# Performance work log

Hardware: AMD Instinct MI355X
Metric: run time of the kernel (lower is better)

## Reference

```python
import jax, jax.numpy as jnp
import numpy as np

B, Lq, C, NH, NP, DFF = 8, 10000, 256, 8, 4, 1024
H_IMG, W_IMG = 100, 100
HD = C // NH


def _layer_norm(x, g, b, eps=1e-5):
    m = jnp.mean(x, -1, keepdims=True)
    v = jnp.mean((x - m) ** 2, -1, keepdims=True)
    return (x - m) / jnp.sqrt(v + eps) * g + b


def _bilinear_sample(value, loc, Hs, Ws):
    # value: [B, Lin, NH, HD]; loc: [B, Lq, NH, NP, 2] normalized to [0,1]
    vt = jnp.transpose(value, (0, 2, 1, 3))  # [B, NH, Lin, HD]
    # move to [B, NH, Lq, NP] layout once; grid_sample(align_corners=False) pixel coords
    x = jnp.transpose(loc[..., 0], (0, 2, 1, 3)) * Ws - 0.5
    y = jnp.transpose(loc[..., 1], (0, 2, 1, 3)) * Hs - 0.5
    x0 = jnp.floor(x); y0 = jnp.floor(y)
    lx = x - x0; ly = y - y0

    def corner(xi, yi, w):
        valid = (xi >= 0) & (xi < Ws) & (yi >= 0) & (yi < Hs)
        xc = jnp.clip(xi, 0, Ws - 1).astype(jnp.int32)
        yc = jnp.clip(yi, 0, Hs - 1).astype(jnp.int32)
        idx = (yc * Ws + xc).reshape(B, NH, Lq * NP, 1)
        v = jnp.take_along_axis(vt, idx, axis=2).reshape(B, NH, Lq, NP, HD)
        return v * (w * valid)[..., None]

    acc = corner(x0, y0, (1 - lx) * (1 - ly))
    acc = acc + corner(x0 + 1, y0, lx * (1 - ly))
    acc = acc + corner(x0, y0 + 1, (1 - lx) * ly)
    acc = acc + corner(x0 + 1, y0 + 1, lx * ly)
    return acc  # [B, NH, Lq, NP, HD]


def setup_inputs() -> dict:
    key = jax.random.key(0)
    ks = jax.random.split(key, 12)
    s = 0.02
    return {
        "query": jax.random.normal(ks[0], (B, Lq, C), jnp.float32),
        "src": jax.random.normal(ks[1], (B, H_IMG * W_IMG, C), jnp.float32),
        "reference_points": jax.random.uniform(ks[2], (B, Lq, 1, 2), jnp.float32),
        "spatial_shapes": jnp.array([[H_IMG, W_IMG]], dtype=jnp.int64),
        "level_start_index": jnp.array([0], dtype=jnp.int64),
        "W_off": jax.random.normal(ks[3], (C, NH * NP * 2), jnp.float32) * s,
        "b_off": jnp.zeros((NH * NP * 2,), jnp.float32),
        "W_aw": jax.random.normal(ks[4], (C, NH * NP), jnp.float32) * s,
        "b_aw": jnp.zeros((NH * NP,), jnp.float32),
        "W_val": jax.random.normal(ks[5], (C, C), jnp.float32) * s,
        "b_val": jnp.zeros((C,), jnp.float32),
        "W_out": jax.random.normal(ks[6], (C, C), jnp.float32) * s,
        "b_out": jnp.zeros((C,), jnp.float32),
        "g1": jnp.ones((C,), jnp.float32),
        "be1": jnp.zeros((C,), jnp.float32),
        "W1": jax.random.normal(ks[7], (C, DFF), jnp.float32) * s,
        "b1": jnp.zeros((DFF,), jnp.float32),
        "W2": jax.random.normal(ks[8], (DFF, C), jnp.float32) * s,
        "b2": jnp.zeros((C,), jnp.float32),
        "g2": jnp.ones((C,), jnp.float32),
        "be2": jnp.zeros((C,), jnp.float32),
    }


def reference(query, src, reference_points, spatial_shapes, level_start_index,
              W_off, b_off, W_aw, b_aw, W_val, b_val, W_out, b_out,
              g1, be1, W1, b1, W2, b2, g2, be2):
    Hs = spatial_shapes[0, 0]
    Ws = spatial_shapes[0, 1]
    # MSDeformAttn (n_levels = 1)
    value = (src @ W_val + b_val).reshape(B, -1, NH, HD)
    off = (query @ W_off + b_off).reshape(B, Lq, NH, NP, 2)
    aw = jax.nn.softmax((query @ W_aw + b_aw).reshape(B, Lq, NH, NP), axis=-1)
    normalizer = jnp.stack([Ws, Hs]).astype(query.dtype)  # (W, H)
    loc = reference_points[:, :, None] + off / normalizer  # [B,Lq,NH,NP,2]
    sampled = _bilinear_sample(value, loc, Hs, Ws)  # [B,NH,Lq,NP,HD]
    attn = jnp.einsum('bhqpd,bqhp->bqhd', sampled, aw).reshape(B, Lq, C)
    attn = attn @ W_out + b_out
    # residual + LN + FFN + LN
    q = _layer_norm(query + attn, g1, be1)
    ffn = jax.nn.relu(q @ W1 + b1) @ W2 + b2
    return _layer_norm(q + ffn, g2, be2)
```

## Files before the change

kernel.cpp:

```cpp
#include <hip/hip_runtime.h>
#include <hip/hip_bf16.h>

typedef __hip_bfloat16 bf16;
typedef unsigned short u16;
typedef short short8 __attribute__((ext_vector_type(8)));
typedef float f32x4 __attribute__((ext_vector_type(4)));

static constexpr int B_   = 8;
static constexpr int Lq_  = 10000;
static constexpr int C_   = 256;
static constexpr int NH_  = 8;
static constexpr int NP_  = 4;
static constexpr int HIMG = 100;
static constexpr int WIMG = 100;
static constexpr int LIN  = 10000;

__device__ __forceinline__ u16 f2bf(float x) {
    union { bf16 b; u16 u; } cv; cv.b = __float2bfloat16(x); return cv.u;
}
__device__ __forceinline__ float bf2f(u16 u) {
    return __uint_as_float((unsigned)u << 16);
}

__device__ __forceinline__ void gl_lds16(const void* g, void* l) {
    __builtin_amdgcn_global_load_lds(
        (const __attribute__((address_space(1))) void*)g,
        (__attribute__((address_space(3))) void*)l, 16, 0, 0);
}
__device__ __forceinline__ void drain_barrier() {
    asm volatile("s_waitcnt vmcnt(0) lgkmcnt(0)" ::: "memory");
    __builtin_amdgcn_s_barrier();
}
#define VMW(N) asm volatile("s_waitcnt vmcnt(" #N ")" ::: "memory")
#define LKW0() asm volatile("s_waitcnt lgkmcnt(0)" ::: "memory")
#define BAR()  __builtin_amdgcn_s_barrier()


template <bool AF32, bool LN>
__global__ __launch_bounds__(512, 2) void gemm256(
    const void* __restrict__ Av, const u16* __restrict__ Bg,
    const float* __restrict__ bias, const float* __restrict__ resid,
    const float* __restrict__ gw, const float* __restrict__ bw,
    u16* __restrict__ Co, int K)
{
    __shared__ __align__(16) u16 At[2][128 * 64];
    __shared__ __align__(16) u16 Bt[2][256 * 64];
    __shared__ float red[2][128][4];

    const int tid  = threadIdx.x;
    const int lane = tid & 63;
    const int w    = tid >> 6;
    const int wm   = w >> 2, wn = w & 3;
    const int m0   = blockIdx.x * 128;

    f32x4 acc[4][4];
#pragma unroll
    for (int i = 0; i < 4; ++i)
#pragma unroll
        for (int j = 0; j < 4; ++j) acc[i][j] = f32x4{0.f, 0.f, 0.f, 0.f};

    auto stageA = [&](int t) {
        const int kt = t << 6;
        if constexpr (AF32) {
            const int row = tid >> 2;
            const int k0  = (tid & 3) << 4;
            const float* s = (const float*)Av + (size_t)(m0 + row) * K + kt + k0;
            float4 v0 = *(const float4*)(s + 0);
            float4 v1 = *(const float4*)(s + 4);
            float4 v2 = *(const float4*)(s + 8);
            float4 v3 = *(const float4*)(s + 12);
            union { short8 s8; u16 u[8]; } ga, gb;
            ga.u[0]=f2bf(v0.x); ga.u[1]=f2bf(v0.y); ga.u[2]=f2bf(v0.z); ga.u[3]=f2bf(v0.w);
            ga.u[4]=f2bf(v1.x); ga.u[5]=f2bf(v1.y); ga.u[6]=f2bf(v1.z); ga.u[7]=f2bf(v1.w);
            gb.u[0]=f2bf(v2.x); gb.u[1]=f2bf(v2.y); gb.u[2]=f2bf(v2.z); gb.u[3]=f2bf(v2.w);
            gb.u[4]=f2bf(v3.x); gb.u[5]=f2bf(v3.y); gb.u[6]=f2bf(v3.z); gb.u[7]=f2bf(v3.w);
            u16* d = &At[t & 1][row * 64];
            *(short8*)&d[(k0)     ^ ((row & 7) << 3)] = ga.s8;
            *(short8*)&d[(k0 + 8) ^ ((row & 7) << 3)] = gb.s8;
        } else {
#pragma unroll
            for (int i = 0; i < 2; ++i) {
                const int rb  = w * 16 + i * 8;
                const int row = rb + (lane >> 3);
                const int gs  = (lane & 7) ^ (row & 7);
                gl_lds16((const u16*)Av + (size_t)(m0 + row) * K + kt + gs * 8,
                         &At[t & 1][rb * 64]);
            }
        }
    };
    auto stageB = [&](int t) {
        const int kt = t << 6;
#pragma unroll
        for (int i = 0; i < 4; ++i) {
            const int rb  = w * 32 + i * 8;
            const int row = rb + (lane >> 3);
            gl_lds16(Bg + (size_t)row * K + kt + (lane & 7) * 8,
                     &Bt[t & 1][rb * 64]);
        }
    };
    auto compute = [&](int t) {
        const u16* a = At[t & 1];
        const u16* b = Bt[t & 1];
#pragma unroll
        for (int ks = 0; ks < 2; ++ks) {
            const int ko = ks * 32 + ((lane >> 4) << 3);
            short8 bfr[4];
#pragma unroll
            for (int n = 0; n < 4; ++n) {
                const int nr = wn * 64 + n * 16 + (lane & 15);
                bfr[n] = *(const short8*)&b[nr * 64 + (ko ^ ((nr & 7) << 3))];
            }
#pragma unroll
            for (int m = 0; m < 4; ++m) {
                const int ar = wm * 64 + m * 16 + (lane & 15);
                const short8 af = *(const short8*)&a[ar * 64 + (ko ^ ((ar & 7) << 3))];
#pragma unroll
                for (int n = 0; n < 4; ++n)
                    acc[m][n] = __builtin_amdgcn_mfma_f32_16x16x32_bf16(
                        af, bfr[n], acc[m][n], 0, 0, 0);
            }
        }
    };

    stageA(0); stageB(0);
    drain_barrier();
    const int nt = K >> 6;
    for (int t = 0; t < nt; ++t) {
        if (t + 1 < nt) { stageA(t + 1); stageB(t + 1); }
        compute(t);
        drain_barrier();
    }

    float bcol[4], gcol[4], becol[4];
#pragma unroll
    for (int n = 0; n < 4; ++n) {
        const int col = wn * 64 + n * 16 + (lane & 15);
        bcol[n] = bias[col];
        if (LN) { gcol[n] = gw[col]; becol[n] = bw[col]; }
    }

    if constexpr (!LN) {
#pragma unroll
        for (int m = 0; m < 4; ++m)
#pragma unroll
            for (int r = 0; r < 4; ++r) {
                const int lr = wm * 64 + m * 16 + (lane >> 4) * 4 + r;
#pragma unroll
                for (int n = 0; n < 4; ++n) {
                    const int col = wn * 64 + n * 16 + (lane & 15);
                    Co[(size_t)(m0 + lr) * 256 + col] = f2bf(acc[m][n][r] + bcol[n]);
                }
            }
    } else {
        float s[4][4], s2[4][4];
#pragma unroll
        for (int m = 0; m < 4; ++m)
#pragma unroll
            for (int r = 0; r < 4; ++r) {
                const int lr = wm * 64 + m * 16 + (lane >> 4) * 4 + r;
                float ps = 0.f, ps2 = 0.f;
#pragma unroll
                for (int n = 0; n < 4; ++n) {
                    const int col = wn * 64 + n * 16 + (lane & 15);
                    float v = acc[m][n][r] + bcol[n]
                            + resid[(size_t)(m0 + lr) * 256 + col];
                    acc[m][n][r] = v;
                    ps += v; ps2 += v * v;
                }
#pragma unroll
                for (int o = 1; o < 16; o <<= 1) {
                    ps  += __shfl_xor(ps,  o);
                    ps2 += __shfl_xor(ps2, o);
                }
                s[m][r] = ps; s2[m][r] = ps2;
            }
        if ((lane & 15) == 0) {
#pragma unroll
            for (int m = 0; m < 4; ++m)
#pragma unroll
                for (int r = 0; r < 4; ++r) {
                    const int lr = wm * 64 + m * 16 + (lane >> 4) * 4 + r;
                    red[0][lr][wn] = s[m][r];
                    red[1][lr][wn] = s2[m][r];
                }
        }
        __syncthreads();
        if (tid < 128) {
            const float ss  = red[0][tid][0] + red[0][tid][1] + red[0][tid][2] + red[0][tid][3];
            const float ss2 = red[1][tid][0] + red[1][tid][1] + red[1][tid][2] + red[1][tid][3];
            const float mean = ss * (1.f / 256.f);
            const float var  = fmaxf(ss2 * (1.f / 256.f) - mean * mean, 0.f);
            red[0][tid][0] = mean;
            red[1][tid][0] = rsqrtf(var + 1e-5f);
        }
        __syncthreads();
#pragma unroll
        for (int m = 0; m < 4; ++m)
#pragma unroll
            for (int r = 0; r < 4; ++r) {
                const int lr = wm * 64 + m * 16 + (lane >> 4) * 4 + r;
                const float mean = red[0][lr][0];
                const float rstd = red[1][lr][0];
#pragma unroll
                for (int n = 0; n < 4; ++n) {
                    const int col = wn * 64 + n * 16 + (lane & 15);
                    const float o = (acc[m][n][r] - mean) * rstd * gcol[n] + becol[n];
                    Co[(size_t)(m0 + lr) * 256 + (col ^ ((lr & 7) << 3))] = f2bf(o);
                }
            }
    }
}

__global__ __launch_bounds__(512) void ffn_fused(
    const u16* __restrict__ q1b, const u16* __restrict__ W1s,
    const u16* __restrict__ W2s, const float* __restrict__ b1,
    const float* __restrict__ b2, const float* __restrict__ g2,
    const float* __restrict__ be2, float* __restrict__ out)
{
    __shared__ __align__(16) u16 As[128 * 256];
    __shared__ __align__(16) u16 Hs[128 * 136];
    __shared__ __align__(16) u16 B1t[3][128 * 32];
    __shared__ __align__(16) u16 B2t[2][256 * 32];
    float (*red)[128][4] = (float (*)[128][4])Hs;

    const int tid  = threadIdx.x;
    const int lane = tid & 63;
    const int w    = tid >> 6;
    const int wm   = w >> 2, wn = w & 3;
    const int m0   = blockIdx.x * 128;

    f32x4 acc2[4][4];
#pragma unroll
    for (int i = 0; i < 4; ++i)
#pragma unroll
        for (int j = 0; j < 4; ++j) acc2[i][j] = f32x4{0.f, 0.f, 0.f, 0.f};

    auto issueB1 = [&](int c, int t, int buf) {
        const int rb  = w * 16;
        const int row = rb + (lane >> 2);
        gl_lds16(W1s + (size_t)(c * 128 + row) * 256 + t * 32 + (lane & 3) * 8,
                 &B1t[buf][rb * 32]);
    };
    auto issueB2 = [&](int c, int u, int buf) {
#pragma unroll
        for (int i = 0; i < 2; ++i) {
            const int rb  = i * 128 + w * 16;
            const int row = rb + (lane >> 2);
            gl_lds16(W2s + (size_t)row * 1024 + c * 128 + u * 32 + (lane & 3) * 8,
                     &B2t[buf][rb * 32]);
        }
    };

#pragma unroll
    for (int i = 0; i < 8; ++i) {
        const int rb = w * 16 + i * 2;
        gl_lds16(q1b + (size_t)(m0 + rb + (lane >> 5)) * 256 + (lane & 31) * 8,
                 &As[rb * 256]);
    }
    issueB1(0, 0, 0); issueB1(0, 1, 1); issueB1(0, 2, 2);
    VMW(2); BAR();

    for (int c = 0; c < 8; ++c) {
        f32x4 acc1[4][2];
#pragma unroll
        for (int i = 0; i < 4; ++i)
#pragma unroll
            for (int j = 0; j < 2; ++j) acc1[i][j] = f32x4{0.f, 0.f, 0.f, 0.f};

        auto g1 = [&](int t, int buf) {
            const u16* bb = B1t[buf];
            const int ko = (lane >> 4) << 3;
            short8 bfr[2];
#pragma unroll
            for (int n = 0; n < 2; ++n) {
                const int nr = wn * 32 + n * 16 + (lane & 15);
                bfr[n] = *(const short8*)&bb[nr * 32 + (ko ^ ((nr & 3) << 3))];
            }
#pragma unroll
            for (int m = 0; m < 4; ++m) {
                const int ar = wm * 64 + m * 16 + (lane & 15);
                const short8 af = *(const short8*)
                    &As[ar * 256 + ((t * 32 + ko) ^ ((ar & 7) << 3))];
#pragma unroll
                for (int n = 0; n < 2; ++n)
                    acc1[m][n] = __builtin_amdgcn_mfma_f32_16x16x32_bf16(
                        af, bfr[n], acc1[m][n], 0, 0, 0);
            }
        };
        auto g2s = [&](int u, int buf) {
            const u16* bb = B2t[buf];
            const int ko = (lane >> 4) << 3;
            short8 bfr[4];
#pragma unroll
            for (int n = 0; n < 4; ++n) {
                const int nr = wn * 64 + n * 16 + (lane & 15);
                bfr[n] = *(const short8*)&bb[nr * 32 + (ko ^ ((nr & 3) << 3))];
            }
#pragma unroll
            for (int m = 0; m < 4; ++m) {
                const int hr = wm * 64 + m * 16 + (lane & 15);
                const short8 af = *(const short8*)&Hs[hr * 136 + u * 32 + ko];
#pragma unroll
                for (int n = 0; n < 4; ++n)
                    acc2[m][n] = __builtin_amdgcn_mfma_f32_16x16x32_bf16(
                        af, bfr[n], acc2[m][n], 0, 0, 0);
            }
        };

        g1(0, 0);
        if (c == 0) { VMW(1); } else { VMW(3); }
        BAR();
        issueB1(c, 3, 0); g1(1, 1); VMW(1); BAR();
        issueB1(c, 4, 1); g1(2, 2); VMW(1); BAR();
        issueB1(c, 5, 2); g1(3, 0); VMW(1); BAR();
        issueB1(c, 6, 0); g1(4, 1); VMW(1); BAR();
        issueB1(c, 7, 1); g1(5, 2); VMW(1); BAR();
        issueB2(c, 0, 0); g1(6, 0); VMW(2); BAR();
        issueB2(c, 1, 1); g1(7, 1); VMW(2); BAR();

#pragma unroll
        for (int n = 0; n < 2; ++n) {
            const int col = wn * 32 + n * 16 + (lane & 15);
            const float bb = b1[c * 128 + col];
#pragma unroll
            for (int m = 0; m < 4; ++m)
#pragma unroll
                for (int r = 0; r < 4; ++r) {
                    const int row = wm * 64 + m * 16 + (lane >> 4) * 4 + r;
                    Hs[row * 136 + col] = f2bf(fmaxf(acc1[m][n][r] + bb, 0.f));
                }
        }
        LKW0(); BAR();

        issueB1(c + 1, 0, 0);                    g2s(0, 0); VMW(1); BAR();
        issueB2(c, 2, 0); issueB1(c + 1, 1, 1);  g2s(1, 1); VMW(1); BAR();
        issueB2(c, 3, 1); issueB1(c + 1, 2, 2);  g2s(2, 0); VMW(1); BAR();
        g2s(3, 1); VMW(6); BAR();
    }
    asm volatile("s_waitcnt vmcnt(0)" ::: "memory");
    BAR();

    float bcol[4], gcol[4], becol[4];
#pragma unroll
    for (int n = 0; n < 4; ++n) {
        const int col = wn * 64 + n * 16 + (lane & 15);
        bcol[n] = b2[col]; gcol[n] = g2[col]; becol[n] = be2[col];
    }
    float s[4][4], s2[4][4];
#pragma unroll
    for (int m = 0; m < 4; ++m)
#pragma unroll
        for (int r = 0; r < 4; ++r) {
            const int lr = wm * 64 + m * 16 + (lane >> 4) * 4 + r;
            float ps = 0.f, ps2 = 0.f;
#pragma unroll
            for (int n = 0; n < 4; ++n) {
                const int col = wn * 64 + n * 16 + (lane & 15);
                const float q = bf2f(As[lr * 256 + (col ^ ((lr & 7) << 3))]);
                const float v = acc2[m][n][r] + bcol[n] + q;
                acc2[m][n][r] = v;
                ps += v; ps2 += v * v;
            }
#pragma unroll
            for (int o = 1; o < 16; o <<= 1) {
                ps  += __shfl_xor(ps,  o);
                ps2 += __shfl_xor(ps2, o);
            }
            s[m][r] = ps; s2[m][r] = ps2;
        }
    if ((lane & 15) == 0) {
#pragma unroll
        for (int m = 0; m < 4; ++m)
#pragma unroll
            for (int r = 0; r < 4; ++r) {
                const int lr = wm * 64 + m * 16 + (lane >> 4) * 4 + r;
                red[0][lr][wn] = s[m][r];
                red[1][lr][wn] = s2[m][r];
            }
    }
    __syncthreads();
    if (tid < 128) {
        const float ss  = red[0][tid][0] + red[0][tid][1] + red[0][tid][2] + red[0][tid][3];
        const float ss2 = red[1][tid][0] + red[1][tid][1] + red[1][tid][2] + red[1][tid][3];
        const float mean = ss * (1.f / 256.f);
        const float var  = fmaxf(ss2 * (1.f / 256.f) - mean * mean, 0.f);
        red[0][tid][0] = mean;
        red[1][tid][0] = rsqrtf(var + 1e-5f);
    }
    __syncthreads();
#pragma unroll
    for (int m = 0; m < 4; ++m)
#pragma unroll
        for (int r = 0; r < 4; ++r) {
            const int lr = wm * 64 + m * 16 + (lane >> 4) * 4 + r;
            const float mean = red[0][lr][0];
            const float rstd = red[1][lr][0];
#pragma unroll
            for (int n = 0; n < 4; ++n) {
                const int col = wn * 64 + n * 16 + (lane & 15);
                out[(size_t)(m0 + lr) * 256 + col] =
                    (acc2[m][n][r] - mean) * rstd * gcol[n] + becol[n];
            }
        }
}

__global__ __launch_bounds__(256) void gemm_oaw(
    const float* __restrict__ Av, const u16* __restrict__ Bt,
    const float* __restrict__ bias, float* __restrict__ C,
    int M, int K, int Nreal, int ldc)
{
    __shared__ __align__(16) u16 Asl[2][128 * 32];
    __shared__ __align__(16) u16 Bsl[2][128 * 32];

    const int tid  = threadIdx.x;
    const int lane = tid & 63;
    const int w    = tid >> 6;
    const int wr   = (w >> 1) * 64;
    const int wc   = (w & 1) * 64;
    const int m0   = blockIdx.y * 128;
    const int n0   = blockIdx.x * 128;

    const int srow = lane >> 2;
    const int scol = (lane & 3) << 3;
    const u16* bG = Bt + (size_t)(n0 + w * 32 + srow) * K + scol;
    const size_t rstep16 = (size_t)16 * K;

    const int ar  = lane >> 3;
    const int ac  = (lane & 7) << 2;
    const float* aGf = Av + (size_t)(m0 + w * 32 + ar) * K + ac;

    const int aRoff = (wr + (lane & 15)) * 32 + (lane >> 4) * 8;
    const int bRoff = (wc + (lane & 15)) * 32 + (lane >> 4) * 8;

    f32x4 acc[4][4];
#pragma unroll
    for (int i = 0; i < 4; ++i)
#pragma unroll
        for (int j = 0; j < 4; ++j) acc[i][j] = f32x4{0.f, 0.f, 0.f, 0.f};

    float4 a4[4];
    const int nt = K >> 5;

#pragma unroll
    for (int rep = 0; rep < 4; ++rep)
        a4[rep] = *(const float4*)(aGf + (size_t)(rep * 8) * K);
#pragma unroll
    for (int rep = 0; rep < 4; ++rep) {
        ushort4 v{f2bf(a4[rep].x), f2bf(a4[rep].y), f2bf(a4[rep].z), f2bf(a4[rep].w)};
        *(ushort4*)&Asl[0][(w * 32 + rep * 8 + ar) * 32 + ac] = v;
    }
    gl_lds16(bG, &Bsl[0][(w * 32) * 32]);
    gl_lds16(bG + rstep16, &Bsl[0][(w * 32 + 16) * 32]);
    drain_barrier();

    for (int t = 0; t < nt; ++t) {
        const int cur = t & 1, nxt = cur ^ 1;
        const int k0n = (t + 1) << 5;
        const bool has_next = (t + 1 < nt);
        if (has_next) {
#pragma unroll
            for (int rep = 0; rep < 4; ++rep)
                a4[rep] = *(const float4*)(aGf + k0n + (size_t)(rep * 8) * K);
            gl_lds16(bG + k0n, &Bsl[nxt][(w * 32) * 32]);
            gl_lds16(bG + k0n + rstep16, &Bsl[nxt][(w * 32 + 16) * 32]);
        }
        short8 af[4], bfr[4];
#pragma unroll
        for (int m = 0; m < 4; ++m) af[m]  = *(const short8*)&Asl[cur][aRoff + m * 16 * 32];
#pragma unroll
        for (int n = 0; n < 4; ++n) bfr[n] = *(const short8*)&Bsl[cur][bRoff + n * 16 * 32];
#pragma unroll
        for (int m = 0; m < 4; ++m)
#pragma unroll
            for (int n = 0; n < 4; ++n)
                acc[m][n] = __builtin_amdgcn_mfma_f32_16x16x32_bf16(
                    af[m], bfr[n], acc[m][n], 0, 0, 0);
        if (has_next) {
#pragma unroll
            for (int rep = 0; rep < 4; ++rep) {
                ushort4 v{f2bf(a4[rep].x), f2bf(a4[rep].y), f2bf(a4[rep].z), f2bf(a4[rep].w)};
                *(ushort4*)&Asl[nxt][(w * 32 + rep * 8 + ar) * 32 + ac] = v;
            }
        }
        drain_barrier();
    }

#pragma unroll
    for (int n = 0; n < 4; ++n) {
        const int gc = n0 + wc + n * 16 + (lane & 15);
        if (gc >= Nreal) continue;
        const float bv = bias[gc];
        const int gr0 = m0 + wr + (lane >> 4) * 4;
#pragma unroll
        for (int m = 0; m < 4; ++m)
#pragma unroll
            for (int r = 0; r < 4; ++r)
                C[(size_t)(gr0 + m * 16 + r) * ldc + gc] = acc[m][n][r] + bv;
    }
}

__global__ __launch_bounds__(256) void prep_all(
    const float* __restrict__ Wv, const float* __restrict__ Wo,
    const float* __restrict__ W1, const float* __restrict__ W2,
    const float* __restrict__ Woff, const float* __restrict__ Waw,
    const float* __restrict__ boff, const float* __restrict__ baw,
    u16* __restrict__ Wvs, u16* __restrict__ Wos,
    u16* __restrict__ W1s, u16* __restrict__ W2s,
    u16* __restrict__ Woa, float* __restrict__ boa)
{
    const int idx = blockIdx.x * 256 + threadIdx.x;
    if (idx < 65536) {
        const int n = idx >> 8, kd = idx & 255;
        Wvs[idx] = f2bf(Wv[(size_t)(kd ^ ((n & 7) << 3)) * 256 + n]);
    } else if (idx < 131072) {
        const int i = idx - 65536, n = i >> 8, kd = i & 255;
        Wos[i] = f2bf(Wo[(size_t)(kd ^ ((n & 7) << 3)) * 256 + n]);
    } else if (idx < 393216) {
        const int i = idx - 131072, n = i >> 8, kd = i & 255;
        W1s[i] = f2bf(W1[(size_t)(kd ^ ((n & 3) << 3)) * 1024 + n]);
    } else if (idx < 655360) {
        const int i = idx - 393216, n = i >> 10, kd = i & 1023;
        W2s[i] = f2bf(W2[(size_t)(kd ^ ((n & 3) << 3)) * 256 + n]);
    } else if (idx < 688128) {
        const int i = idx - 655360, n = i >> 8, k = i & 255;
        float v = 0.f;
        if (n < 64)      v = Woff[(size_t)k * 64 + n];
        else if (n < 96) v = Waw[(size_t)k * 32 + (n - 64)];
        Woa[i] = f2bf(v);
    } else if (idx < 688256) {
        const int i = idx - 688128;
        boa[i] = (i < 64) ? boff[i] : (i < 96 ? baw[i - 64] : 0.f);
    }
}

__global__ __launch_bounds__(256) void sample_attn(
    const u16* __restrict__ val, const float* __restrict__ oaw,
    const float* __restrict__ refp, u16* __restrict__ attn)
{
    const int t   = threadIdx.x;
    const int gid = blockIdx.x * 64 + (t >> 2);
    const int c0  = (t & 3) << 3;
    const int h   = gid & (NH_ - 1);
    const int bq  = gid >> 3;

    const float* row = oaw + (size_t)bq * 96;
    const float rx = refp[(size_t)bq * 2 + 0] * (float)WIMG;
    const float ry = refp[(size_t)bq * 2 + 1] * (float)HIMG;

    const float4 aw4 = *(const float4*)(row + 64 + h * 4);
    const float mx = fmaxf(fmaxf(aw4.x, aw4.y), fmaxf(aw4.z, aw4.w));
    const float e0 = __expf(aw4.x - mx), e1 = __expf(aw4.y - mx);
    const float e2 = __expf(aw4.z - mx), e3 = __expf(aw4.w - mx);
    const float inv = 1.f / (e0 + e1 + e2 + e3);
    const float w4[4] = {e0 * inv, e1 * inv, e2 * inv, e3 * inv};

    const int b = bq / Lq_;
    const u16* vb = val + (size_t)b * LIN * C_ + h * 32 + c0;

    float acc[8] = {};
#pragma unroll
    for (int p = 0; p < NP_; ++p) {
        const float2 off = *(const float2*)(row + (h * 4 + p) * 2);
        const float x = rx + off.x - 0.5f;
        const float y = ry + off.y - 0.5f;
        const float xf = floorf(x), yf = floorf(y);
        const float lx = x - xf, ly = y - yf;
        const int x0 = (int)xf, y0 = (int)yf;
        const float wp = w4[p];
        const float w00 = wp * (1.f - lx) * (1.f - ly);
        const float w10 = wp * lx * (1.f - ly);
        const float w01 = wp * (1.f - lx) * ly;
        const float w11 = wp * lx * ly;

#pragma unroll
        for (int c = 0; c < 4; ++c) {
            const int xi = x0 + (c & 1);
            const int yi = y0 + (c >> 1);
            const float wc = (c == 0) ? w00 : (c == 1) ? w10 : (c == 2) ? w01 : w11;
            const bool v = ((unsigned)xi < (unsigned)WIMG) & ((unsigned)yi < (unsigned)HIMG);
            const int idx = v ? (yi * WIMG + xi) : 0;
            const float w = v ? wc : 0.f;
            const short8 d = *(const short8*)(vb + (size_t)idx * C_);
#pragma unroll
            for (int j = 0; j < 8; ++j)
                acc[j] = fmaf(w, bf2f(((const u16*)&d)[j]), acc[j]);
        }
    }

    union { short8 s; u16 u[8]; } o;
#pragma unroll
    for (int j = 0; j < 8; ++j) o.u[j] = f2bf(acc[j]);
    *(short8*)(attn + (size_t)bq * C_ + h * 32 + c0) = o.s;
}

extern "C" void kernel_launch(void* const* d_in, const int* in_sizes, int n_in,
                              void* d_out, int out_size, void* d_ws, size_t ws_size,
                              hipStream_t stream)
{
    const float* query = (const float*)d_in[0];
    const float* src   = (const float*)d_in[1];
    const float* refp  = (const float*)d_in[2];
    const float* W_off = (const float*)d_in[5];
    const float* b_off = (const float*)d_in[6];
    const float* W_aw  = (const float*)d_in[7];
    const float* b_aw  = (const float*)d_in[8];
    const float* W_val = (const float*)d_in[9];
    const float* b_val = (const float*)d_in[10];
    const float* W_out = (const float*)d_in[11];
    const float* b_out = (const float*)d_in[12];
    const float* g1    = (const float*)d_in[13];
    const float* be1   = (const float*)d_in[14];
    const float* W1    = (const float*)d_in[15];
    const float* b1    = (const float*)d_in[16];
    const float* W2    = (const float*)d_in[17];
    const float* b2    = (const float*)d_in[18];
    const float* g2    = (const float*)d_in[19];
    const float* be2   = (const float*)d_in[20];
    float* out = (float*)d_out;

    char* ws = (char*)d_ws;
    const int R = B_ * Lq_;

    u16*  val  = (u16*)(ws + 0);
    float* oaw = (float*)(ws + 40960000);
    u16*  attn = (u16*)(ws + 71680000);
    u16*  q1b  = (u16*)(ws + 112640000);
    u16*  Wvs  = (u16*)(ws + 153600000);
    u16*  Wos  = (u16*)(ws + 153600000 + 131072);
    u16*  W1s  = (u16*)(ws + 153600000 + 262144);
    u16*  W2s  = (u16*)(ws + 153600000 + 786432);
    u16*  Woa  = (u16*)(ws + 153600000 + 1310720);
    float* boa = (float*)(ws + 153600000 + 1376256);

    prep_all<<<2689, 256, 0, stream>>>(W_val, W_out, W1, W2, W_off, W_aw,
                                       b_off, b_aw, Wvs, Wos, W1s, W2s,
                                       Woa, boa);

    gemm256<true, false><<<625, 512, 0, stream>>>(
        src, Wvs, b_val, nullptr, nullptr, nullptr, val, 256);

    gemm_oaw<<<dim3(1, 625), 256, 0, stream>>>(
        query, Woa, boa, oaw, R, 256, 96, 96);

    sample_attn<<<10000, 256, 0, stream>>>(val, oaw, refp, attn);

    gemm256<false, true><<<625, 512, 0, stream>>>(
        attn, Wos, b_out, query, g1, be1, q1b, 256);

    ffn_fused<<<625, 512, 0, stream>>>(q1b, W1s, W2s, b1, b2, g2, be2, out);
}
```

Baseline: 310.9 us.

## Pre-tile FFN weights into contiguous 8KB tiles and unify triple-buffered pipeline

The weight prep now writes W1 and W2 as contiguous 4096-element pre-swizzled tiles, so each weight-tile load is a single contiguous 16-byte-per-lane global-to-LDS copy instead of strided row loads. The FFN kernel now runs one uniform triple-buffered pipeline across both GEMM phases, splitting W2 into 16 half-width tiles per chunk so load granularity matches W1. It also hoists per-lane address math and raises wave priority with s_setprio around the MFMA bursts. The aim is to cut load-issue overhead and pipeline stalls, at the cost of more barriers in the second GEMM and a more intricate prefetch schedule.

After: 374.3 us. 1.2x slower.

```diff
diff --git a/kernel.cpp b/kernel.cpp
--- a/kernel.cpp
+++ b/kernel.cpp
@@ -34,7 +34,6 @@
 #define VMW(N) asm volatile("s_waitcnt vmcnt(" #N ")" ::: "memory")
 #define LKW0() asm volatile("s_waitcnt lgkmcnt(0)" ::: "memory")
 #define BAR()  __builtin_amdgcn_s_barrier()
-
 
 template <bool AF32, bool LN>
 __global__ __launch_bounds__(512, 2) void gemm256(
@@ -212,15 +211,15 @@
 }
 
 __global__ __launch_bounds__(512) void ffn_fused(
-    const u16* __restrict__ q1b, const u16* __restrict__ W1s,
-    const u16* __restrict__ W2s, const float* __restrict__ b1,
-    const float* __restrict__ b2, const float* __restrict__ g2,
+    const u16* __restrict__ q1b, const u16* __restrict__ W1t,
+    const u16* __restrict__ W2t, const float* __restrict__ b1,
+    const float* __restrict__ b2, const float* __restrict__ g2w,
     const float* __restrict__ be2, float* __restrict__ out)
 {
     __shared__ __align__(16) u16 As[128 * 256];
     __shared__ __align__(16) u16 Hs[128 * 136];
-    __shared__ __align__(16) u16 B1t[3][128 * 32];
-    __shared__ __align__(16) u16 B2t[2][256 * 32];
+    __shared__ __align__(16) u16 B1s[3][4096];
+    __shared__ __align__(16) u16 B2s[3][4096];
     float (*red)[128][4] = (float (*)[128][4])Hs;
 
     const int tid  = threadIdx.x;
@@ -228,6 +227,21 @@
     const int w    = tid >> 6;
     const int wm   = w >> 2, wn = w & 3;
     const int m0   = blockIdx.x * 128;
+    const int ko   = (lane >> 4) << 3;
+
+    int bfb[2];
+#pragma unroll
+    for (int q = 0; q < 2; ++q) {
+        const int nr = wn * 32 + q * 16 + (lane & 15);
+        const int pr = nr >> 1;
+        bfb[q] = pr * 64 + (nr & 1) * 32 + (ko ^ ((pr & 3) << 3));
+    }
+    int arow[4], aswz[4], hrow[4];
+#pragma unroll
+    for (int m = 0; m < 4; ++m) {
+        const int ar = wm * 64 + m * 16 + (lane & 15);
+        arow[m] = ar * 256; aswz[m] = (ar & 7) << 3; hrow[m] = ar * 136;
+    }
 
     f32x4 acc2[4][4];
 #pragma unroll
@@ -235,20 +249,11 @@
 #pragma unroll
         for (int j = 0; j < 4; ++j) acc2[i][j] = f32x4{0.f, 0.f, 0.f, 0.f};
 
-    auto issueB1 = [&](int c, int t, int buf) {
-        const int rb  = w * 16;
-        const int row = rb + (lane >> 2);
-        gl_lds16(W1s + (size_t)(c * 128 + row) * 256 + t * 32 + (lane & 3) * 8,
-                 &B1t[buf][rb * 32]);
+    auto issueB1 = [&](int tile, int buf) {
+        gl_lds16(W1t + (size_t)tile * 4096 + w * 512 + lane * 8, &B1s[buf][w * 512]);
     };
-    auto issueB2 = [&](int c, int u, int buf) {
-#pragma unroll
-        for (int i = 0; i < 2; ++i) {
-            const int rb  = i * 128 + w * 16;
-            const int row = rb + (lane >> 2);
-            gl_lds16(W2s + (size_t)row * 1024 + c * 128 + u * 32 + (lane & 3) * 8,
-                     &B2t[buf][rb * 32]);
-        }
+    auto issueB2 = [&](int tile, int buf) {
+        gl_lds16(W2t + (size_t)tile * 4096 + w * 512 + lane * 8, &B2s[buf][w * 512]);
     };
 
 #pragma unroll
@@ -257,10 +262,11 @@
         gl_lds16(q1b + (size_t)(m0 + rb + (lane >> 5)) * 256 + (lane & 31) * 8,
                  &As[rb * 256]);
     }
-    issueB1(0, 0, 0); issueB1(0, 1, 1); issueB1(0, 2, 2);
-    VMW(2); BAR();
+    issueB1(0, 0); issueB1(1, 1);
+    VMW(1); BAR();
 
     for (int c = 0; c < 8; ++c) {
+        const int bb = c * 8;
         f32x4 acc1[4][2];
 #pragma unroll
         for (int i = 0; i < 4; ++i)
@@ -268,74 +274,90 @@
             for (int j = 0; j < 2; ++j) acc1[i][j] = f32x4{0.f, 0.f, 0.f, 0.f};
 
         auto g1 = [&](int t, int buf) {
-            const u16* bb = B1t[buf];
-            const int ko = (lane >> 4) << 3;
             short8 bfr[2];
 #pragma unroll
-            for (int n = 0; n < 2; ++n) {
-                const int nr = wn * 32 + n * 16 + (lane & 15);
-                bfr[n] = *(const short8*)&bb[nr * 32 + (ko ^ ((nr & 3) << 3))];
-            }
+            for (int q = 0; q < 2; ++q)
+                bfr[q] = *(const short8*)&B1s[buf][bfb[q]];
+            __builtin_amdgcn_s_setprio(1);
 #pragma unroll
             for (int m = 0; m < 4; ++m) {
-                const int ar = wm * 64 + m * 16 + (lane & 15);
                 const short8 af = *(const short8*)
-                    &As[ar * 256 + ((t * 32 + ko) ^ ((ar & 7) << 3))];
-#pragma unroll
-                for (int n = 0; n < 2; ++n)
-                    acc1[m][n] = __builtin_amdgcn_mfma_f32_16x16x32_bf16(
-                        af, bfr[n], acc1[m][n], 0, 0, 0);
-            }
+                    &As[arow[m] + ((t * 32 + ko) ^ aswz[m])];
+#pragma unroll
+                for (int q = 0; q < 2; ++q)
+                    acc1[m][q] = __builtin_amdgcn_mfma_f32_16x16x32_bf16(
+                        af, bfr[q], acc1[m][q], 0, 0, 0);
+            }
+            __builtin_amdgcn_s_setprio(0);
         };
-        auto g2s = [&](int u, int buf) {
-            const u16* bb = B2t[buf];
-            const int ko = (lane >> 4) << 3;
-            short8 bfr[4];
-#pragma unroll
-            for (int n = 0; n < 4; ++n) {
-                const int nr = wn * 64 + n * 16 + (lane & 15);
-                bfr[n] = *(const short8*)&bb[nr * 32 + (ko ^ ((nr & 3) << 3))];
-            }
-#pragma unroll
-            for (int m = 0; m < 4; ++m) {
-                const int hr = wm * 64 + m * 16 + (lane & 15);
-                const short8 af = *(const short8*)&Hs[hr * 136 + u * 32 + ko];
-#pragma unroll
-                for (int n = 0; n < 4; ++n)
-                    acc2[m][n] = __builtin_amdgcn_mfma_f32_16x16x32_bf16(
-                        af, bfr[n], acc2[m][n], 0, 0, 0);
-            }
-        };
-
-        g1(0, 0);
-        if (c == 0) { VMW(1); } else { VMW(3); }
-        BAR();
-        issueB1(c, 3, 0); g1(1, 1); VMW(1); BAR();
-        issueB1(c, 4, 1); g1(2, 2); VMW(1); BAR();
-        issueB1(c, 5, 2); g1(3, 0); VMW(1); BAR();
-        issueB1(c, 6, 0); g1(4, 1); VMW(1); BAR();
-        issueB1(c, 7, 1); g1(5, 2); VMW(1); BAR();
-        issueB2(c, 0, 0); g1(6, 0); VMW(2); BAR();
-        issueB2(c, 1, 1); g1(7, 1); VMW(2); BAR();
-
-#pragma unroll
-        for (int n = 0; n < 2; ++n) {
-            const int col = wn * 32 + n * 16 + (lane & 15);
-            const float bb = b1[c * 128 + col];
+
+#pragma unroll
+        for (int t = 0; t < 6; ++t) {
+            issueB1(bb + t + 2, (bb + t + 2) % 3);
+            g1(t, (bb + t) % 3);
+            VMW(1); BAR();
+        }
+        issueB2(bb + 0, (bb + 0) % 3); g1(6, (bb + 6) % 3); VMW(1); BAR();
+        issueB2(bb + 1, (bb + 1) % 3); g1(7, (bb + 7) % 3); VMW(1); BAR();
+
+#pragma unroll
+        for (int q = 0; q < 2; ++q) {
+            const int col = wn * 32 + q * 16 + (lane & 15);
+            const float bv = b1[c * 128 + col];
 #pragma unroll
             for (int m = 0; m < 4; ++m)
 #pragma unroll
                 for (int r = 0; r < 4; ++r) {
                     const int row = wm * 64 + m * 16 + (lane >> 4) * 4 + r;
-                    Hs[row * 136 + col] = f2bf(fmaxf(acc1[m][n][r] + bb, 0.f));
+                    Hs[row * 136 + col] = f2bf(fmaxf(acc1[m][q][r] + bv, 0.f));
                 }
         }
         LKW0(); BAR();
 
-        issueB1(c + 1, 0, 0);                    g2s(0, 0); VMW(1); BAR();
-        issueB2(c, 2, 0); issueB1(c + 1, 1, 1);  g2s(1, 1); VMW(1); BAR();
-        issueB2(c, 3, 1); issueB1(c + 1, 2, 2);  g2s(2, 0); VMW(1); BAR();
-        g2s(3, 1); VMW(6); BAR();
+#pragma unroll
+        for (int j = 0; j < 6; ++j) {
+            issueB2(bb + j + 2, (bb + j + 2) % 3);
+            {
+                const int ku = j >> 1, nh = j & 1;
+                short8 bfr[2];
+#pragma unroll
+                for (int q = 0; q < 2; ++q)
+                    bfr[q] = *(const short8*)&B2s[(bb + j) % 3][bfb[q]];
+                __builtin_amdgcn_s_setprio(1);
+#pragma unroll
+                for (int m = 0; m < 4; ++m) {
+                    const short8 af = *(const short8*)&Hs[hrow[m] + ku * 32 + ko];
+#pragma unroll
+                    for (int q = 0; q < 2; ++q)
+                        acc2[m][2 * nh + q] = __builtin_amdgcn_mfma_f32_16x16x32_bf16(
+                            af, bfr[q], acc2[m][2 * nh + q], 0, 0, 0);
+                }
+                __builtin_amdgcn_s_setprio(0);
+            }
+            VMW(1); BAR();
+        }
+#pragma unroll
+        for (int j = 6; j < 8; ++j) {
+            issueB1(c < 7 ? bb + 8 + (j - 6) : (j - 6), (bb + 8 + (j - 6)) % 3);
+            {
+                const int ku = j >> 1, nh = j & 1;
+                short8 bfr[2];
+#pragma unroll
+                for (int q = 0; q < 2; ++q)
+                    bfr[q] = *(const short8*)&B2s[(bb + j) % 3][bfb[q]];
+                __builtin_amdgcn_s_setprio(1);
+#pragma unroll
+                for (int m = 0; m < 4; ++m) {
+                    const short8 af = *(const short8*)&Hs[hrow[m] + ku * 32 + ko];
+#pragma unroll
+                    for (int q = 0; q < 2; ++q)
+                        acc2[m][2 * nh + q] = __builtin_amdgcn_mfma_f32_16x16x32_bf16(
+                            af, bfr[q], acc2[m][2 * nh + q], 0, 0, 0);
+                }
+                __builtin_amdgcn_s_setprio(0);
+            }
+            VMW(1); BAR();
+        }
     }
     asm volatile("s_waitcnt vmcnt(0)" ::: "memory");
     BAR();
@@ -344,7 +366,7 @@
 #pragma unroll
     for (int n = 0; n < 4; ++n) {
         const int col = wn * 64 + n * 16 + (lane & 15);
-        bcol[n] = b2[col]; gcol[n] = g2[col]; becol[n] = be2[col];
+        bcol[n] = b2[col]; gcol[n] = g2w[col]; becol[n] = be2[col];
     }
     float s[4][4], s2[4][4];
 #pragma unroll
@@ -505,7 +527,7 @@
     const float* __restrict__ Woff, const float* __restrict__ Waw,
     const float* __restrict__ boff, const float* __restrict__ baw,
     u16* __restrict__ Wvs, u16* __restrict__ Wos,
-    u16* __restrict__ W1s, u16* __restrict__ W2s,
+    u16* __restrict__ W1t, u16* __restrict__ W2t,
     u16* __restrict__ Woa, float* __restrict__ boa)
 {
     const int idx = blockIdx.x * 256 + threadIdx.x;
@@ -516,11 +538,23 @@
         const int i = idx - 65536, n = i >> 8, kd = i & 255;
         Wos[i] = f2bf(Wo[(size_t)(kd ^ ((n & 7) << 3)) * 256 + n]);
     } else if (idx < 393216) {
-        const int i = idx - 131072, n = i >> 8, kd = i & 255;
-        W1s[i] = f2bf(W1[(size_t)(kd ^ ((n & 3) << 3)) * 1024 + n]);
+        const int i = idx - 131072;
+        const int tile = i >> 12, si = i & 4095;
+        const int c = tile >> 3, t = tile & 7;
+        const int pr = si >> 6, inner = si & 63;
+        const int nr = (pr << 1) | (inner >> 5);
+        const int kk = (inner & 31) ^ ((pr & 3) << 3);
+        W1t[i] = f2bf(W1[(size_t)(t * 32 + kk) * 1024 + c * 128 + nr]);
     } else if (idx < 655360) {
-        const int i = idx - 393216, n = i >> 10, kd = i & 1023;
-        W2s[i] = f2bf(W2[(size_t)(kd ^ ((n & 3) << 3)) * 256 + n]);
+        const int i = idx - 393216;
+        const int tile = i >> 12, si = i & 4095;
+        const int c = tile >> 3, j = tile & 7;
+        const int ku = j >> 1, nh = j & 1;
+        const int pr = si >> 6, inner = si & 63;
+        const int rl = (pr << 1) | (inner >> 5);
+        const int kk = (inner & 31) ^ ((pr & 3) << 3);
+        const int n = ((rl >> 5) << 6) + (nh << 5) + (rl & 31);
+        W2t[i] = f2bf(W2[(size_t)(c * 128 + ku * 32 + kk) * 256 + n]);
     } else if (idx < 688128) {
         const int i = idx - 655360, n = i >> 8, k = i & 255;
         float v = 0.f;
@@ -627,13 +661,13 @@
     u16*  q1b  = (u16*)(ws + 112640000);
     u16*  Wvs  = (u16*)(ws + 153600000);
     u16*  Wos  = (u16*)(ws + 153600000 + 131072);
-    u16*  W1s  = (u16*)(ws + 153600000 + 262144);
-    u16*  W2s  = (u16*)(ws + 153600000 + 786432);
+    u16*  W1t  = (u16*)(ws + 153600000 + 262144);
+    u16*  W2t  = (u16*)(ws + 153600000 + 786432);
     u16*  Woa  = (u16*)(ws + 153600000 + 1310720);
     float* boa = (float*)(ws + 153600000 + 1376256);
 
     prep_all<<<2689, 256, 0, stream>>>(W_val, W_out, W1, W2, W_off, W_aw,
-                                       b_off, b_aw, Wvs, Wos, W1s, W2s,
+                                       b_off, b_aw, Wvs, Wos, W1t, W2t,
                                        Woa, boa);
 
     gemm256<true, false><<<625, 512, 0, stream>>>(
@@ -647,5 +681,5 @@
     gemm256<false, true><<<625, 512, 0, stream>>>(
         attn, Wos, b_out, query, g1, be1, q1b, 256);
 
-    ffn_fused<<<625, 512, 0, stream>>>(q1b, W1s, W2s, b1, b2, g2, be2, out);
-}
+    ffn_fused<<<625, 512, 0, stream>>>(q1b, W1t, W2t, b1, b2, g2, be2, out);
+}
```

## Halve GEMM K-tile to 32 with paired-row LDS layout for higher occupancy

Applied to the files above, without the earlier changes.

The 256-wide GEMM kernel now stages K in tiles of 32 instead of 64, which halves the LDS footprint per block. The launch bound rises to allow 4 blocks per CU. Shared-memory tiles use a new layout that packs row pairs with an XOR swizzle. The weight prep kernel pre-tiles W_val and W_out into that exact per-tile order, so the B operand becomes one contiguous block load per K-step. The trade-off is twice as many barrier/drain iterations per GEMM, in exchange for more resident waves to hide memory latency.

Measured after the change: 321.3 us. 1.03x slower.

```diff
diff --git a/kernel.cpp b/kernel.cpp
--- a/kernel.cpp
+++ b/kernel.cpp
@@ -36,15 +36,15 @@
 #define BAR()  __builtin_amdgcn_s_barrier()
 
 
-template <bool AF32, bool LN>
-__global__ __launch_bounds__(512, 2) void gemm256(
+template <int AMODE, int EPI>
+__global__ __launch_bounds__(512, 4) void gemm256(
     const void* __restrict__ Av, const u16* __restrict__ Bg,
     const float* __restrict__ bias, const float* __restrict__ resid,
     const float* __restrict__ gw, const float* __restrict__ bw,
-    u16* __restrict__ Co, int K)
+    u16* __restrict__ Co, int K, int ldc)
 {
-    __shared__ __align__(16) u16 At[2][128 * 64];
-    __shared__ __align__(16) u16 Bt[2][256 * 64];
+    __shared__ __align__(16) u16 At[2][128 * 32];
+    __shared__ __align__(16) u16 Bt[2][256 * 32];
     __shared__ float red[2][128][4];
 
     const int tid  = threadIdx.x;
@@ -60,71 +60,61 @@
         for (int j = 0; j < 4; ++j) acc[i][j] = f32x4{0.f, 0.f, 0.f, 0.f};
 
     auto stageA = [&](int t) {
-        const int kt = t << 6;
-        if constexpr (AF32) {
-            const int row = tid >> 2;
-            const int k0  = (tid & 3) << 4;
-            const float* s = (const float*)Av + (size_t)(m0 + row) * K + kt + k0;
-            float4 v0 = *(const float4*)(s + 0);
-            float4 v1 = *(const float4*)(s + 4);
-            float4 v2 = *(const float4*)(s + 8);
-            float4 v3 = *(const float4*)(s + 12);
-            union { short8 s8; u16 u[8]; } ga, gb;
-            ga.u[0]=f2bf(v0.x); ga.u[1]=f2bf(v0.y); ga.u[2]=f2bf(v0.z); ga.u[3]=f2bf(v0.w);
-            ga.u[4]=f2bf(v1.x); ga.u[5]=f2bf(v1.y); ga.u[6]=f2bf(v1.z); ga.u[7]=f2bf(v1.w);
-            gb.u[0]=f2bf(v2.x); gb.u[1]=f2bf(v2.y); gb.u[2]=f2bf(v2.z); gb.u[3]=f2bf(v2.w);
-            gb.u[4]=f2bf(v3.x); gb.u[5]=f2bf(v3.y); gb.u[6]=f2bf(v3.z); gb.u[7]=f2bf(v3.w);
-            u16* d = &At[t & 1][row * 64];
-            *(short8*)&d[(k0)     ^ ((row & 7) << 3)] = ga.s8;
-            *(short8*)&d[(k0 + 8) ^ ((row & 7) << 3)] = gb.s8;
+        const int kt = t << 5;
+        if constexpr (AMODE == 0) {
+            const int pr = tid >> 3;
+            const int h  = (tid >> 2) & 1;
+            const int ge = (tid & 3) ^ (pr & 3);
+            const float* s = (const float*)Av
+                + (size_t)(m0 + (pr << 1) + h) * K + kt + ge * 8;
+            const float4 v0 = *(const float4*)(s + 0);
+            const float4 v1 = *(const float4*)(s + 4);
+            union { short8 s8; u16 u[8]; } g;
+            g.u[0]=f2bf(v0.x); g.u[1]=f2bf(v0.y); g.u[2]=f2bf(v0.z); g.u[3]=f2bf(v0.w);
+            g.u[4]=f2bf(v1.x); g.u[5]=f2bf(v1.y); g.u[6]=f2bf(v1.z); g.u[7]=f2bf(v1.w);
+            *(short8*)&At[t & 1][tid * 8] = g.s8;
         } else {
-#pragma unroll
-            for (int i = 0; i < 2; ++i) {
-                const int rb  = w * 16 + i * 8;
-                const int row = rb + (lane >> 3);
-                const int gs  = (lane & 7) ^ (row & 7);
-                gl_lds16((const u16*)Av + (size_t)(m0 + row) * K + kt + gs * 8,
-                         &At[t & 1][rb * 64]);
-            }
+            const int pr = w * 8 + (lane >> 3);
+            const int h  = (lane >> 2) & 1;
+            const int ge = (lane & 3) ^ (pr & 3);
+            gl_lds16((const u16*)Av + (size_t)(m0 + (pr << 1) + h) * K + kt + ge * 8,
+                     &At[t & 1][w * 512]);
         }
     };
     auto stageB = [&](int t) {
-        const int kt = t << 6;
-#pragma unroll
-        for (int i = 0; i < 4; ++i) {
-            const int rb  = w * 32 + i * 8;
-            const int row = rb + (lane >> 3);
-            gl_lds16(Bg + (size_t)row * K + kt + (lane & 7) * 8,
-                     &Bt[t & 1][rb * 64]);
+#pragma unroll
+        for (int i = 0; i < 2; ++i) {
+            const int sb = w * 1024 + i * 512;
+            gl_lds16(Bg + (size_t)t * 8192 + sb + lane * 8, &Bt[t & 1][sb]);
         }
     };
     auto compute = [&](int t) {
         const u16* a = At[t & 1];
         const u16* b = Bt[t & 1];
-#pragma unroll
-        for (int ks = 0; ks < 2; ++ks) {
-            const int ko = ks * 32 + ((lane >> 4) << 3);
-            short8 bfr[4];
-#pragma unroll
-            for (int n = 0; n < 4; ++n) {
-                const int nr = wn * 64 + n * 16 + (lane & 15);
-                bfr[n] = *(const short8*)&b[nr * 64 + (ko ^ ((nr & 7) << 3))];
-            }
-#pragma unroll
-            for (int m = 0; m < 4; ++m) {
-                const int ar = wm * 64 + m * 16 + (lane & 15);
-                const short8 af = *(const short8*)&a[ar * 64 + (ko ^ ((ar & 7) << 3))];
-#pragma unroll
-                for (int n = 0; n < 4; ++n)
-                    acc[m][n] = __builtin_amdgcn_mfma_f32_16x16x32_bf16(
-                        af, bfr[n], acc[m][n], 0, 0, 0);
-            }
+        const int ko = (lane >> 4) << 3;
+        short8 bfr[4];
+#pragma unroll
+        for (int n = 0; n < 4; ++n) {
+            const int nr = wn * 64 + n * 16 + (lane & 15);
+            const int pr = nr >> 1;
+            bfr[n] = *(const short8*)&b[pr * 64 + (nr & 1) * 32 + (ko ^ ((pr & 3) << 3))];
+        }
+#pragma unroll
+        for (int m = 0; m < 4; ++m) {
+            const int ar = wm * 64 + m * 16 + (lane & 15);
+            const int pa = ar >> 1;
+            const short8 af = *(const short8*)
+                &a[pa * 64 + (ar & 1) * 32 + (ko ^ ((pa & 3) << 3))];
+#pragma unroll
+            for (int n = 0; n < 4; ++n)
+                acc[m][n] = __builtin_amdgcn_mfma_f32_16x16x32_bf16(
+                    af, bfr[n], acc[m][n], 0, 0, 0);
         }
     };
 
     stageA(0); stageB(0);
     drain_barrier();
-    const int nt = K >> 6;
+    const int nt = K >> 5;
     for (int t = 0; t < nt; ++t) {
         if (t + 1 < nt) { stageA(t + 1); stageB(t + 1); }
         compute(t);
@@ -136,10 +126,10 @@
     for (int n = 0; n < 4; ++n) {
         const int col = wn * 64 + n * 16 + (lane & 15);
         bcol[n] = bias[col];
-        if (LN) { gcol[n] = gw[col]; becol[n] = bw[col]; }
-    }
-
-    if constexpr (!LN) {
+        if (EPI == 2) { gcol[n] = gw[col]; becol[n] = bw[col]; }
+    }
+
+    if constexpr (EPI == 0) {
 #pragma unroll
         for (int m = 0; m < 4; ++m)
 #pragma unroll
@@ -148,7 +138,7 @@
 #pragma unroll
                 for (int n = 0; n < 4; ++n) {
                     const int col = wn * 64 + n * 16 + (lane & 15);
-                    Co[(size_t)(m0 + lr) * 256 + col] = f2bf(acc[m][n][r] + bcol[n]);
+                    Co[(size_t)(m0 + lr) * ldc + col] = f2bf(acc[m][n][r] + bcol[n]);
                 }
             }
     } else {
@@ -163,7 +153,7 @@
                 for (int n = 0; n < 4; ++n) {
                     const int col = wn * 64 + n * 16 + (lane & 15);
                     float v = acc[m][n][r] + bcol[n]
-                            + resid[(size_t)(m0 + lr) * 256 + col];
+                            + ((const float*)resid)[(size_t)(m0 + lr) * 256 + col];
                     acc[m][n][r] = v;
                     ps += v; ps2 += v * v;
                 }
@@ -510,11 +500,18 @@
 {
     const int idx = blockIdx.x * 256 + threadIdx.x;
     if (idx < 65536) {
-        const int n = idx >> 8, kd = idx & 255;
-        Wvs[idx] = f2bf(Wv[(size_t)(kd ^ ((n & 7) << 3)) * 256 + n]);
+        const int t = idx >> 13, si = idx & 8191;
+        const int pr = si >> 6, h = (si >> 5) & 1, e = si & 31;
+        const int n = (pr << 1) | h;
+        const int k = t * 32 + (e ^ ((pr & 3) << 3));
+        Wvs[idx] = f2bf(Wv[(size_t)k * 256 + n]);
     } else if (idx < 131072) {
-        const int i = idx - 65536, n = i >> 8, kd = i & 255;
-        Wos[i] = f2bf(Wo[(size_t)(kd ^ ((n & 7) << 3)) * 256 + n]);
+        const int i = idx - 65536;
+        const int t = i >> 13, si = i & 8191;
+        const int pr = si >> 6, h = (si >> 5) & 1, e = si & 31;
+        const int n = (pr << 1) | h;
+        const int k = t * 32 + (e ^ ((pr & 3) << 3));
+        Wos[i] = f2bf(Wo[(size_t)k * 256 + n]);
     } else if (idx < 393216) {
         const int i = idx - 131072, n = i >> 8, kd = i & 255;
         W1s[i] = f2bf(W1[(size_t)(kd ^ ((n & 3) << 3)) * 1024 + n]);
@@ -636,16 +633,16 @@
                                        b_off, b_aw, Wvs, Wos, W1s, W2s,
                                        Woa, boa);
 
-    gemm256<true, false><<<625, 512, 0, stream>>>(
-        src, Wvs, b_val, nullptr, nullptr, nullptr, val, 256);
+    gemm256<0, 0><<<625, 512, 0, stream>>>(
+        src, Wvs, b_val, nullptr, nullptr, nullptr, val, 256, 256);
 
     gemm_oaw<<<dim3(1, 625), 256, 0, stream>>>(
         query, Woa, boa, oaw, R, 256, 96, 96);
 
     sample_attn<<<10000, 256, 0, stream>>>(val, oaw, refp, attn);
 
-    gemm256<false, true><<<625, 512, 0, stream>>>(
-        attn, Wos, b_out, query, g1, be1, q1b, 256);
+    gemm256<1, 2><<<625, 512, 0, stream>>>(
+        attn, Wos, b_out, query, g1, be1, q1b, 256, 256);
 
     ffn_fused<<<625, 512, 0, stream>>>(q1b, W1s, W2s, b1, b2, g2, be2, out);
 }
```
